# Optimization experiments

Measured on AMD Instinct MI355X. Metric: run time of the kernel, lower is better.

The kernel has to match this reference:

```python
import jax, jax.numpy as jnp
import numpy as np

N_NODES = 50000
N_RAND_EDGES = 800000
IN_FEATS = 128
NUM_HEADS = 4
OUT_FEATS = 32
NEG_SLOPE = 0.2


def setup_inputs() -> dict:
    key = jax.random.key(0)
    k_feat, k_src, k_dst, k_w, k_al, k_ar, k_b = jax.random.split(key, 7)
    feat = jax.random.normal(k_feat, (N_NODES, IN_FEATS), dtype=jnp.float32)
    # random edges + self-loops so every node has in-degree >= 1 (DGL requirement)
    src_r = jax.random.randint(k_src, (N_RAND_EDGES,), 0, N_NODES)
    dst_r = jax.random.randint(k_dst, (N_RAND_EDGES,), 0, N_NODES)
    loops = jnp.arange(N_NODES, dtype=src_r.dtype)
    src = jnp.concatenate([src_r, loops]).astype(jnp.int64)
    dst = jnp.concatenate([dst_r, loops]).astype(jnp.int64)
    W = jax.random.normal(k_w, (NUM_HEADS * OUT_FEATS, IN_FEATS), dtype=jnp.float32) * 0.05
    attn_l = jax.random.normal(k_al, (1, NUM_HEADS, OUT_FEATS), dtype=jnp.float32) * 0.1
    attn_r = jax.random.normal(k_ar, (1, NUM_HEADS, OUT_FEATS), dtype=jnp.float32) * 0.1
    bias = jnp.zeros((NUM_HEADS * OUT_FEATS,), dtype=jnp.float32)
    return {"feat": feat, "src": src, "dst": dst, "W": W,
            "attn_l": attn_l, "attn_r": attn_r, "bias": bias}


def _gat_forward(feat, src, dst, W, attn_l, attn_r, bias):
    n = feat.shape[0]
    # shared projection: in homogeneous path feat_src2 = feat_dst2 = fc(h)
    ft = (feat @ W.T).reshape(n, NUM_HEADS, OUT_FEATS)       # [N,H,D]
    el = jnp.sum(ft * attn_l, axis=-1)                        # [N,H]
    er = jnp.sum(ft * attn_r, axis=-1)                        # [N,H]
    e = el[src] + er[dst]                                     # [E,H]
    e = jnp.where(e > 0, e, NEG_SLOPE * e)                    # leaky_relu
    # edge softmax per destination node (numerically stable)
    m = jax.ops.segment_max(e, dst, num_segments=n)           # [N,H]
    ex = jnp.exp(e - m[dst])
    s = jax.ops.segment_sum(ex, dst, num_segments=n)          # [N,H]
    a = ex / s[dst]                                           # [E,H]
    # u_mul_e -> sum : attention-weighted aggregation
    msg1 = ft[src] * a[:, :, None]                            # [E,H,D]
    initial_ft = jax.ops.segment_sum(msg1, dst, num_segments=n)
    # u_mul_v -> sum : elementwise src*dst product aggregation
    msg2 = ft[src] * ft[dst]                                  # [E,H,D]
    add_ft = jax.ops.segment_sum(msg2, dst, num_segments=n)
    rst = initial_ft + add_ft + bias.reshape(1, NUM_HEADS, OUT_FEATS)
    return rst


def reference(feat, src, dst, W, attn_l, attn_r, bias):
    return _gat_forward(feat, src, dst, W, attn_l, attn_r, bias)
```

## Files before the change

### kernel.cpp

```cpp
#include <hip/hip_runtime.h>
#include <hip/hip_bf16.h>

#define IN_FEATS 128
#define HD 128
#define NEG_SLOPE 0.2f
#define LDR 128
#define CAP 64
#define BINW 256
#define CAPB 5120
#define NBLK 256
#define GPB 8
#define NPG 32
#define GM 64
#define LDA 136

typedef short s8v __attribute__((ext_vector_type(8)));
typedef float f4v __attribute__((ext_vector_type(4)));
typedef float f2v __attribute__((ext_vector_type(2)));

static __device__ __forceinline__ unsigned short f2bf(float f) {
    unsigned int u = __float_as_uint(f);
    unsigned int r = (u + 0x7FFFu + ((u >> 16) & 1u)) >> 16;
    return (unsigned short)r;
}
static __device__ __forceinline__ float bf2f(unsigned short h) {
    return __uint_as_float(((unsigned int)h) << 16);
}

static __device__ __forceinline__ void stage_W(unsigned short (*Wb)[LDA],
                                               const float* __restrict__ W) {
    const float4* W4 = (const float4*)W;
    for (int i = threadIdx.x; i < 4096; i += 256) {
        int r = i >> 5, q = i & 31;
        float4 w = W4[i];
        ushort4 o;
        o.x = f2bf(w.x); o.y = f2bf(w.y); o.z = f2bf(w.z); o.w = f2bf(w.w);
        *(ushort4*)&Wb[r][q * 4] = o;
    }
}

static __device__ __forceinline__ void gemm_tile(
        unsigned short (*Wb)[LDA], unsigned short (*Ab)[LDA],
        const float* __restrict__ feat, const float* __restrict__ attn_l,
        const float* __restrict__ attn_r, unsigned short* __restrict__ ftb,
        float* __restrict__ el, float* __restrict__ er, int N, int rbase) {
    const int tid  = threadIdx.x;
    const int wave = tid >> 6;
    const int lane = tid & 63;
    const int m    = lane & 15;
    const int quad = lane >> 4;

    const float4* F4 = (const float4*)feat;
    for (int i = tid; i < 2048; i += 256) {
        int r = i >> 5, q = i & 31;
        int gr = rbase + r;
        float4 v = (gr < N) ? F4[(size_t)gr * 32 + q]
                            : make_float4(0.f, 0.f, 0.f, 0.f);
        ushort4 o;
        o.x = f2bf(v.x); o.y = f2bf(v.y); o.z = f2bf(v.z); o.w = f2bf(v.w);
        *(ushort4*)&Ab[r][q * 4] = o;
    }
    __syncthreads();

    f4v acc[8];
#pragma unroll
    for (int t = 0; t < 8; ++t) acc[t] = (f4v){0.f, 0.f, 0.f, 0.f};

    const int arow = wave * 16 + m;
#pragma unroll
    for (int k0 = 0; k0 < 4; ++k0) {
        s8v a = *(const s8v*)&Ab[arow][k0 * 32 + quad * 8];
#pragma unroll
        for (int t = 0; t < 8; ++t) {
            s8v b = *(const s8v*)&Wb[t * 16 + m][k0 * 32 + quad * 8];
            acc[t] = __builtin_amdgcn_mfma_f32_16x16x32_bf16(a, b, acc[t], 0, 0, 0);
        }
    }

#pragma unroll
    for (int reg = 0; reg < 4; ++reg) {
        int gr = rbase + wave * 16 + quad * 4 + reg;
        if (gr < N) {
            unsigned short* dstrow = &ftb[(size_t)gr * LDR];
#pragma unroll
            for (int t = 0; t < 8; ++t)
                dstrow[t * 16 + m] = f2bf(acc[t][reg]);
        }
    }

    float al[8], ar[8];
#pragma unroll
    for (int t = 0; t < 8; ++t) {
        al[t] = attn_l[t * 16 + m];
        ar[t] = attn_r[t * 16 + m];
    }
#pragma unroll
    for (int h = 0; h < 4; ++h) {
#pragma unroll
        for (int reg = 0; reg < 4; ++reg) {
            float pl = acc[2 * h][reg] * al[2 * h] + acc[2 * h + 1][reg] * al[2 * h + 1];
            float pr = acc[2 * h][reg] * ar[2 * h] + acc[2 * h + 1][reg] * ar[2 * h + 1];
            pl += __shfl_xor(pl, 1); pr += __shfl_xor(pr, 1);
            pl += __shfl_xor(pl, 2); pr += __shfl_xor(pr, 2);
            pl += __shfl_xor(pl, 4); pr += __shfl_xor(pr, 4);
            pl += __shfl_xor(pl, 8); pr += __shfl_xor(pr, 8);
            if (m == 0) {
                int gr = rbase + wave * 16 + quad * 4 + reg;
                if (gr < N) {
                    el[gr * 4 + h] = pl;
                    er[gr * 4 + h] = pr;
                }
            }
        }
    }
}

__global__ __launch_bounds__(256) void count_gemm(
        const float* __restrict__ feat, const float* __restrict__ W,
        const float* __restrict__ attn_l, const float* __restrict__ attn_r,
        const int* __restrict__ dst, int E, int* __restrict__ cntBB,
        unsigned short* __restrict__ ftb, float* __restrict__ el,
        float* __restrict__ er, int N, int nbins) {
    __shared__ __align__(16) char smem[52224];
    const int tid = threadIdx.x;
    if (blockIdx.x < NBLK) {
        int* hist = (int*)smem;
        hist[tid] = 0;
        __syncthreads();
        const int chunk = (E + NBLK - 1) / NBLK;
        const int base = blockIdx.x * chunk;
        const int end = min(base + chunk, E);
        for (int i = base + tid; i < end; i += 256)
            atomicAdd(&hist[dst[i] >> 8], 1);
        __syncthreads();
        cntBB[blockIdx.x * 256 + tid] = hist[tid];
        return;
    }
    unsigned short (*Wb)[LDA] = (unsigned short (*)[LDA])smem;
    unsigned short (*Ab)[LDA] = (unsigned short (*)[LDA])(smem + 128 * LDA * 2);
    stage_W(Wb, W);
    gemm_tile(Wb, Ab, feat, attn_l, attn_r, ftb, el, er, N,
              (blockIdx.x - NBLK) * GM);
}

__global__ __launch_bounds__(256) void scan_scatter(
        const int* __restrict__ src, const int* __restrict__ dst, int E,
        const int* __restrict__ cntBB, unsigned int* __restrict__ binbuf,
        int nbins) {
    __shared__ int obase[256];
    __shared__ int lcnt[256];
    const int tid = threadIdx.x;
    const int bid = blockIdx.x;
    {
        int acc0 = 0, acc1 = 0, acc2 = 0, acc3 = 0;
        int acc4 = 0, acc5 = 0, acc6 = 0, acc7 = 0;
        int b = 0;
        for (; b + 8 <= bid; b += 8) {
            acc0 += cntBB[(b + 0) * 256 + tid];
            acc1 += cntBB[(b + 1) * 256 + tid];
            acc2 += cntBB[(b + 2) * 256 + tid];
            acc3 += cntBB[(b + 3) * 256 + tid];
            acc4 += cntBB[(b + 4) * 256 + tid];
            acc5 += cntBB[(b + 5) * 256 + tid];
            acc6 += cntBB[(b + 6) * 256 + tid];
            acc7 += cntBB[(b + 7) * 256 + tid];
        }
        for (; b < bid; ++b) acc0 += cntBB[b * 256 + tid];
        obase[tid] = ((acc0 + acc1) + (acc2 + acc3)) + ((acc4 + acc5) + (acc6 + acc7));
    }
    lcnt[tid] = 0;
    __syncthreads();
    const int chunk = (E + NBLK - 1) / NBLK;
    const int base = bid * chunk;
    const int end = min(base + chunk, E);
    for (int i = base + tid; i < end; i += 256) {
        int d = dst[i];
        int s = src[i];
        int bin = d >> 8;
        int r = atomicAdd(&lcnt[bin], 1);
        int idx = obase[bin] + r;
        if (idx < CAPB)
            binbuf[(size_t)bin * CAPB + idx] =
                ((unsigned int)(d & 255) << 16) | (unsigned int)s;
    }
}

__global__ __launch_bounds__(256) void bucket_agg(
        const unsigned int* __restrict__ binbuf, const int* __restrict__ cntBB,
        const unsigned short* __restrict__ ftb, const float* __restrict__ el,
        const float* __restrict__ er, const float* __restrict__ bias,
        float* __restrict__ out, int N, int nbins) {
    const int bin = blockIdx.x >> 3;
    const int g   = blockIdx.x & (GPB - 1);
    const int tid = threadIdx.x;

    __shared__ unsigned short lb[NPG * CAP];
    __shared__ int lcnt[NPG];
    __shared__ int red[256];

    if (tid < NPG) lcnt[tid] = 0;
    red[tid] = cntBB[tid * 256 + bin];
    __syncthreads();
    for (int s = 128; s > 0; s >>= 1) {
        if (tid < s) red[tid] += red[tid + s];
        __syncthreads();
    }
    const int total = min(red[0], CAPB);

    const unsigned int* bb = binbuf + (size_t)bin * CAPB;
    for (int i = tid; i < total; i += 256) {
        unsigned int v = bb[i];
        int dl = (int)(v >> 16);
        if ((dl >> 5) == g) {
            int ln = dl & (NPG - 1);
            int pos = atomicAdd(&lcnt[ln], 1);
            if (pos < CAP) lb[(ln << 6) + pos] = (unsigned short)(v & 0xFFFFu);
        }
    }
    __syncthreads();

    const int wave = tid >> 6;
    const int lane = tid & 63;
    const int h  = lane >> 4;
    const int c0 = lane * 2;

    for (int ln = wave; ln < NPG; ln += 4) {
        const int n = (bin << 8) + (g << 5) + ln;
        if (n >= N) break;

        const float ern = er[(n << 2) + h];
        unsigned int tn = *(const unsigned int*)(ftb + ((size_t)n << 7) + c0);
        f2v ftn; ftn.x = __uint_as_float(tn << 16);
        ftn.y = __uint_as_float(tn & 0xFFFF0000u);

        const int deg = min(lcnt[ln], CAP);
        const unsigned short* eb = &lb[ln << 6];

        f2v accA = (f2v){0.f, 0.f};
        f2v accB = (f2v){0.f, 0.f};
        float sum = 0.f;

        int i = 0;
        for (; i + 4 <= deg; i += 4) {
            ushort4 s4 = *(const ushort4*)&eb[i];
            int sA = s4.x, sB = s4.y, sC = s4.z, sD = s4.w;
            float eA = el[(sA << 2) + h];
            float eB = el[(sB << 2) + h];
            float eC = el[(sC << 2) + h];
            float eD = el[(sD << 2) + h];
            unsigned int fA = *(const unsigned int*)(ftb + ((size_t)sA << 7) + c0);
            unsigned int fB = *(const unsigned int*)(ftb + ((size_t)sB << 7) + c0);
            unsigned int fC = *(const unsigned int*)(ftb + ((size_t)sC << 7) + c0);
            unsigned int fD = *(const unsigned int*)(ftb + ((size_t)sD << 7) + c0);
            eA += ern; eB += ern; eC += ern; eD += ern;
            eA = fmaxf(eA, NEG_SLOPE * eA);
            eB = fmaxf(eB, NEG_SLOPE * eB);
            eC = fmaxf(eC, NEG_SLOPE * eC);
            eD = fmaxf(eD, NEG_SLOPE * eD);
            float xA = __expf(eA), xB = __expf(eB);
            float xC = __expf(eC), xD = __expf(eD);
            f2v ffA; ffA.x = __uint_as_float(fA << 16); ffA.y = __uint_as_float(fA & 0xFFFF0000u);
            f2v ffB; ffB.x = __uint_as_float(fB << 16); ffB.y = __uint_as_float(fB & 0xFFFF0000u);
            f2v ffC; ffC.x = __uint_as_float(fC << 16); ffC.y = __uint_as_float(fC & 0xFFFF0000u);
            f2v ffD; ffD.x = __uint_as_float(fD << 16); ffD.y = __uint_as_float(fD & 0xFFFF0000u);
            sum += (xA + xB) + (xC + xD);
            accA += xA * ffA;
            accA += xB * ffB;
            accA += xC * ffC;
            accA += xD * ffD;
            accB += ffA + ffB;
            accB += ffC + ffD;
        }
        for (; i < deg; ++i) {
            int s = eb[i];
            float e = el[(s << 2) + h] + ern;
            e = fmaxf(e, NEG_SLOPE * e);
            float x = __expf(e);
            unsigned int f = *(const unsigned int*)(ftb + ((size_t)s << 7) + c0);
            f2v ff; ff.x = __uint_as_float(f << 16); ff.y = __uint_as_float(f & 0xFFFF0000u);
            sum += x;
            accA += x * ff;
            accB += ff;
        }

        float inv = 1.f / sum;
        f2v o = accA * inv + ftn * accB;
        float2 ov;
        ov.x = o.x + bias[c0];
        ov.y = o.y + bias[c0 + 1];
        *(float2*)(out + (size_t)n * HD + c0) = ov;
    }
}

extern "C" void kernel_launch(void* const* d_in, const int* in_sizes, int n_in,
                              void* d_out, int out_size, void* d_ws, size_t ws_size,
                              hipStream_t stream) {
    const float* feat   = (const float*)d_in[0];
    const int*   src    = (const int*)d_in[1];
    const int*   dst    = (const int*)d_in[2];
    const float* W      = (const float*)d_in[3];
    const float* attn_l = (const float*)d_in[4];
    const float* attn_r = (const float*)d_in[5];
    const float* bias   = (const float*)d_in[6];

    const int N = in_sizes[0] / IN_FEATS;
    const int E = in_sizes[1];
    const int nbins = (N + BINW - 1) / BINW;

    char* p = (char*)d_ws;
    auto alloc = [&](size_t bytes) {
        char* q = p;
        p += (bytes + 255) & ~(size_t)255;
        return q;
    };
    unsigned short* ftb  = (unsigned short*)alloc((size_t)N * LDR * 2);
    float* el      = (float*)alloc((size_t)N * 4 * 4);
    float* er      = (float*)alloc((size_t)N * 4 * 4);
    unsigned int* binbuf = (unsigned int*)alloc((size_t)nbins * CAPB * 4);
    int*   cntBB   = (int*)alloc((size_t)NBLK * 256 * 4);

    const int gemm_blocks = (N + GM - 1) / GM;
    count_gemm<<<NBLK + gemm_blocks, 256, 0, stream>>>(
        feat, W, attn_l, attn_r, dst, E, cntBB, ftb, el, er, N, nbins);

    scan_scatter<<<NBLK, 256, 0, stream>>>(src, dst, E, cntBB, binbuf, nbins);

    bucket_agg<<<nbins * GPB, 256, 0, stream>>>(binbuf, cntBB, ftb, el, er,
                                                bias, (float*)d_out, N, nbins);
}
```

Before: 168.5 us.

## Software-pipeline edge gathers in batches of 8 with padded dummy node

Pads each destination's neighbor list to a multiple of 8 using a dummy node whose features are zero and whose logit is very negative. The aggregation loop then prefetches the next 8 edges while processing the current 8. Per-bin totals are computed once in the scatter kernel instead of reduced in every aggregation block, and the per-block histogram is stored as 16-bit. The aim is more memory-level parallelism on the random gathers, at the cost of extra register pressure and some wasted padded work.

```diff
diff --git a/kernel.cpp b/kernel.cpp
--- a/kernel.cpp
+++ b/kernel.cpp
@@ -22,9 +22,6 @@
     unsigned int u = __float_as_uint(f);
     unsigned int r = (u + 0x7FFFu + ((u >> 16) & 1u)) >> 16;
     return (unsigned short)r;
-}
-static __device__ __forceinline__ float bf2f(unsigned short h) {
-    return __uint_as_float(((unsigned int)h) << 16);
 }
 
 static __device__ __forceinline__ void stage_W(unsigned short (*Wb)[LDA],
@@ -118,7 +115,7 @@
 __global__ __launch_bounds__(256) void count_gemm(
         const float* __restrict__ feat, const float* __restrict__ W,
         const float* __restrict__ attn_l, const float* __restrict__ attn_r,
-        const int* __restrict__ dst, int E, int* __restrict__ cntBB,
+        const int* __restrict__ dst, int E, unsigned short* __restrict__ cntBB,
         unsigned short* __restrict__ ftb, float* __restrict__ el,
         float* __restrict__ er, int N, int nbins) {
     __shared__ __align__(16) char smem[52224];
@@ -133,8 +130,12 @@
         for (int i = base + tid; i < end; i += 256)
             atomicAdd(&hist[dst[i] >> 8], 1);
         __syncthreads();
-        cntBB[blockIdx.x * 256 + tid] = hist[tid];
+        cntBB[blockIdx.x * 256 + tid] = (unsigned short)hist[tid];
         return;
+    }
+    if (blockIdx.x == NBLK) {
+        if (tid < 64) ((unsigned int*)(ftb + (size_t)N * LDR))[tid] = 0u;
+        if (tid < 4)  el[N * 4 + tid] = -1e30f;
     }
     unsigned short (*Wb)[LDA] = (unsigned short (*)[LDA])smem;
     unsigned short (*Ab)[LDA] = (unsigned short (*)[LDA])(smem + 128 * LDA * 2);
@@ -145,8 +146,8 @@
 
 __global__ __launch_bounds__(256) void scan_scatter(
         const int* __restrict__ src, const int* __restrict__ dst, int E,
-        const int* __restrict__ cntBB, unsigned int* __restrict__ binbuf,
-        int nbins) {
+        const unsigned short* __restrict__ cntBB, unsigned int* __restrict__ binbuf,
+        int* __restrict__ binTotal, int nbins) {
     __shared__ int obase[256];
     __shared__ int lcnt[256];
     const int tid = threadIdx.x;
@@ -183,10 +184,50 @@
             binbuf[(size_t)bin * CAPB + idx] =
                 ((unsigned int)(d & 255) << 16) | (unsigned int)s;
     }
-}
-
-__global__ __launch_bounds__(256) void bucket_agg(
-        const unsigned int* __restrict__ binbuf, const int* __restrict__ cntBB,
+    __syncthreads();
+    if (bid == NBLK - 1)
+        binTotal[tid] = obase[tid] + lcnt[tid];
+}
+
+struct B8 {
+    float e[8];
+    unsigned int f[8];
+};
+
+static __device__ __forceinline__ B8 loadb(const unsigned short* eb, int base,
+                                           const float* __restrict__ el,
+                                           const unsigned int* __restrict__ ftbu,
+                                           int h, int lane) {
+    B8 r;
+    ushort4 q0 = *(const ushort4*)&eb[base];
+    ushort4 q1 = *(const ushort4*)&eb[base + 4];
+    unsigned int id[8] = {q0.x, q0.y, q0.z, q0.w, q1.x, q1.y, q1.z, q1.w};
+#pragma unroll
+    for (int j = 0; j < 8; ++j) {
+        r.e[j] = el[(id[j] << 2) + h];
+        r.f[j] = ftbu[(id[j] << 6) + lane];
+    }
+    return r;
+}
+
+static __device__ __forceinline__ void procb(const B8& v, float ern, float& sum,
+                                             f2v& accA, f2v& accB) {
+#pragma unroll
+    for (int j = 0; j < 8; ++j) {
+        float e = v.e[j] + ern;
+        e = fmaxf(e, NEG_SLOPE * e);
+        float x = __expf(e);
+        f2v ff;
+        ff.x = __uint_as_float(v.f[j] << 16);
+        ff.y = __uint_as_float(v.f[j] & 0xFFFF0000u);
+        sum += x;
+        accA += x * ff;
+        accB += ff;
+    }
+}
+
+__global__ __launch_bounds__(256, 8) void bucket_agg(
+        const unsigned int* __restrict__ binbuf, const int* __restrict__ binTotal,
         const unsigned short* __restrict__ ftb, const float* __restrict__ el,
         const float* __restrict__ er, const float* __restrict__ bias,
         float* __restrict__ out, int N, int nbins) {
@@ -196,16 +237,11 @@
 
     __shared__ unsigned short lb[NPG * CAP];
     __shared__ int lcnt[NPG];
-    __shared__ int red[256];
 
     if (tid < NPG) lcnt[tid] = 0;
-    red[tid] = cntBB[tid * 256 + bin];
-    __syncthreads();
-    for (int s = 128; s > 0; s >>= 1) {
-        if (tid < s) red[tid] += red[tid + s];
-        __syncthreads();
-    }
-    const int total = min(red[0], CAPB);
+    __syncthreads();
+
+    const int total = min(binTotal[bin], CAPB);
 
     const unsigned int* bb = binbuf + (size_t)bin * CAPB;
     for (int i = tid; i < total; i += 256) {
@@ -218,69 +254,50 @@
         }
     }
     __syncthreads();
+    if (tid < NPG) {
+        int c = min(lcnt[tid], CAP);
+        int cp = (c + 7) & ~7;
+        for (int k = c; k < cp; ++k) lb[(tid << 6) + k] = (unsigned short)N;
+        lcnt[tid] = cp;
+    }
+    __syncthreads();
 
     const int wave = tid >> 6;
     const int lane = tid & 63;
     const int h  = lane >> 4;
     const int c0 = lane * 2;
+    const unsigned int* ftbu = (const unsigned int*)ftb;
 
     for (int ln = wave; ln < NPG; ln += 4) {
         const int n = (bin << 8) + (g << 5) + ln;
         if (n >= N) break;
 
         const float ern = er[(n << 2) + h];
-        unsigned int tn = *(const unsigned int*)(ftb + ((size_t)n << 7) + c0);
+        unsigned int tn = ftbu[((unsigned int)n << 6) + lane];
         f2v ftn; ftn.x = __uint_as_float(tn << 16);
         ftn.y = __uint_as_float(tn & 0xFFFF0000u);
 
-        const int deg = min(lcnt[ln], CAP);
+        const int nb = lcnt[ln] >> 3;
         const unsigned short* eb = &lb[ln << 6];
 
         f2v accA = (f2v){0.f, 0.f};
         f2v accB = (f2v){0.f, 0.f};
         float sum = 0.f;
 
-        int i = 0;
-        for (; i + 4 <= deg; i += 4) {
-            ushort4 s4 = *(const ushort4*)&eb[i];
-            int sA = s4.x, sB = s4.y, sC = s4.z, sD = s4.w;
-            float eA = el[(sA << 2) + h];
-            float eB = el[(sB << 2) + h];
-            float eC = el[(sC << 2) + h];
-            float eD = el[(sD << 2) + h];
-            unsigned int fA = *(const unsigned int*)(ftb + ((size_t)sA << 7) + c0);
-            unsigned int fB = *(const unsigned int*)(ftb + ((size_t)sB << 7) + c0);
-            unsigned int fC = *(const unsigned int*)(ftb + ((size_t)sC << 7) + c0);
-            unsigned int fD = *(const unsigned int*)(ftb + ((size_t)sD << 7) + c0);
-            eA += ern; eB += ern; eC += ern; eD += ern;
-            eA = fmaxf(eA, NEG_SLOPE * eA);
-            eB = fmaxf(eB, NEG_SLOPE * eB);
-            eC = fmaxf(eC, NEG_SLOPE * eC);
-            eD = fmaxf(eD, NEG_SLOPE * eD);
-            float xA = __expf(eA), xB = __expf(eB);
-            float xC = __expf(eC), xD = __expf(eD);
-            f2v ffA; ffA.x = __uint_as_float(fA << 16); ffA.y = __uint_as_float(fA & 0xFFFF0000u);
-            f2v ffB; ffB.x = __uint_as_float(fB << 16); ffB.y = __uint_as_float(fB & 0xFFFF0000u);
-            f2v ffC; ffC.x = __uint_as_float(fC << 16); ffC.y = __uint_as_float(fC & 0xFFFF0000u);
-            f2v ffD; ffD.x = __uint_as_float(fD << 16); ffD.y = __uint_as_float(fD & 0xFFFF0000u);
-            sum += (xA + xB) + (xC + xD);
-            accA += xA * ffA;
-            accA += xB * ffB;
-            accA += xC * ffC;
-            accA += xD * ffD;
-            accB += ffA + ffB;
-            accB += ffC + ffD;
-        }
-        for (; i < deg; ++i) {
-            int s = eb[i];
-            float e = el[(s << 2) + h] + ern;
-            e = fmaxf(e, NEG_SLOPE * e);
-            float x = __expf(e);
-            unsigned int f = *(const unsigned int*)(ftb + ((size_t)s << 7) + c0);
-            f2v ff; ff.x = __uint_as_float(f << 16); ff.y = __uint_as_float(f & 0xFFFF0000u);
-            sum += x;
-            accA += x * ff;
-            accB += ff;
+        if (nb > 0) {
+            B8 A = loadb(eb, 0, el, ftbu, h, lane);
+            int b = 0;
+            while (true) {
+                if (b + 1 < nb) {
+                    B8 Bn = loadb(eb, (b + 1) << 3, el, ftbu, h, lane);
+                    procb(A, ern, sum, accA, accB);
+                    A = Bn;
+                    ++b;
+                } else {
+                    procb(A, ern, sum, accA, accB);
+                    break;
+                }
+            }
         }
 
         float inv = 1.f / sum;
@@ -313,18 +330,20 @@
         p += (bytes + 255) & ~(size_t)255;
         return q;
     };
-    unsigned short* ftb  = (unsigned short*)alloc((size_t)N * LDR * 2);
-    float* el      = (float*)alloc((size_t)N * 4 * 4);
-    float* er      = (float*)alloc((size_t)N * 4 * 4);
+    unsigned short* ftb  = (unsigned short*)alloc((size_t)(N + 1) * LDR * 2);
+    float* el      = (float*)alloc((size_t)(N + 1) * 4 * 4);
+    float* er      = (float*)alloc((size_t)(N + 1) * 4 * 4);
     unsigned int* binbuf = (unsigned int*)alloc((size_t)nbins * CAPB * 4);
-    int*   cntBB   = (int*)alloc((size_t)NBLK * 256 * 4);
+    unsigned short* cntBB = (unsigned short*)alloc((size_t)NBLK * 256 * 2);
+    int* binTotal  = (int*)alloc((size_t)nbins * 4);
 
     const int gemm_blocks = (N + GM - 1) / GM;
     count_gemm<<<NBLK + gemm_blocks, 256, 0, stream>>>(
         feat, W, attn_l, attn_r, dst, E, cntBB, ftb, el, er, N, nbins);
 
-    scan_scatter<<<NBLK, 256, 0, stream>>>(src, dst, E, cntBB, binbuf, nbins);
-
-    bucket_agg<<<nbins * GPB, 256, 0, stream>>>(binbuf, cntBB, ftb, el, er,
+    scan_scatter<<<NBLK, 256, 0, stream>>>(src, dst, E, cntBB, binbuf,
+                                           binTotal, nbins);
+
+    bucket_agg<<<nbins * GPB, 256, 0, stream>>>(binbuf, binTotal, ftb, el, er,
                                                 bias, (float*)d_out, N, nbins);
 }
```

After: 169.7 us. Within noise of the previous version (+0.7%).

## Precompute bin totals in scatter, halve nodes per aggregation block, shrink counts

Applied to the files above, without the earlier changes.

The last scatter block now writes per-bin totals, so each aggregation block reads one value instead of reducing 256 counts from cntBB. Per-block histogram counts are stored as 16-bit values to cut traffic in the scan. The aggregation grid doubles to 16 groups per bin with 16 nodes each, which raises parallelism but means every bin's edge list is scanned twice as many times. Gather indexing switches to 32-bit unsigned word offsets to simplify address arithmetic.

```diff
diff --git a/kernel.cpp b/kernel.cpp
--- a/kernel.cpp
+++ b/kernel.cpp
@@ -9,8 +9,8 @@
 #define BINW 256
 #define CAPB 5120
 #define NBLK 256
-#define GPB 8
-#define NPG 32
+#define GPB 16
+#define NPG 16
 #define GM 64
 #define LDA 136
 
@@ -22,9 +22,6 @@
     unsigned int u = __float_as_uint(f);
     unsigned int r = (u + 0x7FFFu + ((u >> 16) & 1u)) >> 16;
     return (unsigned short)r;
-}
-static __device__ __forceinline__ float bf2f(unsigned short h) {
-    return __uint_as_float(((unsigned int)h) << 16);
 }
 
 static __device__ __forceinline__ void stage_W(unsigned short (*Wb)[LDA],
@@ -118,7 +115,7 @@
 __global__ __launch_bounds__(256) void count_gemm(
         const float* __restrict__ feat, const float* __restrict__ W,
         const float* __restrict__ attn_l, const float* __restrict__ attn_r,
-        const int* __restrict__ dst, int E, int* __restrict__ cntBB,
+        const int* __restrict__ dst, int E, unsigned short* __restrict__ cntBB,
         unsigned short* __restrict__ ftb, float* __restrict__ el,
         float* __restrict__ er, int N, int nbins) {
     __shared__ __align__(16) char smem[52224];
@@ -133,7 +130,7 @@
         for (int i = base + tid; i < end; i += 256)
             atomicAdd(&hist[dst[i] >> 8], 1);
         __syncthreads();
-        cntBB[blockIdx.x * 256 + tid] = hist[tid];
+        cntBB[blockIdx.x * 256 + tid] = (unsigned short)hist[tid];
         return;
     }
     unsigned short (*Wb)[LDA] = (unsigned short (*)[LDA])smem;
@@ -145,8 +142,8 @@
 
 __global__ __launch_bounds__(256) void scan_scatter(
         const int* __restrict__ src, const int* __restrict__ dst, int E,
-        const int* __restrict__ cntBB, unsigned int* __restrict__ binbuf,
-        int nbins) {
+        const unsigned short* __restrict__ cntBB, unsigned int* __restrict__ binbuf,
+        int* __restrict__ binTotal, int nbins) {
     __shared__ int obase[256];
     __shared__ int lcnt[256];
     const int tid = threadIdx.x;
@@ -183,35 +180,33 @@
             binbuf[(size_t)bin * CAPB + idx] =
                 ((unsigned int)(d & 255) << 16) | (unsigned int)s;
     }
+    __syncthreads();
+    if (bid == NBLK - 1)
+        binTotal[tid] = obase[tid] + lcnt[tid];
 }
 
 __global__ __launch_bounds__(256) void bucket_agg(
-        const unsigned int* __restrict__ binbuf, const int* __restrict__ cntBB,
+        const unsigned int* __restrict__ binbuf, const int* __restrict__ binTotal,
         const unsigned short* __restrict__ ftb, const float* __restrict__ el,
         const float* __restrict__ er, const float* __restrict__ bias,
         float* __restrict__ out, int N, int nbins) {
-    const int bin = blockIdx.x >> 3;
+    const int bin = blockIdx.x >> 4;
     const int g   = blockIdx.x & (GPB - 1);
     const int tid = threadIdx.x;
 
     __shared__ unsigned short lb[NPG * CAP];
     __shared__ int lcnt[NPG];
-    __shared__ int red[256];
 
     if (tid < NPG) lcnt[tid] = 0;
-    red[tid] = cntBB[tid * 256 + bin];
-    __syncthreads();
-    for (int s = 128; s > 0; s >>= 1) {
-        if (tid < s) red[tid] += red[tid + s];
-        __syncthreads();
-    }
-    const int total = min(red[0], CAPB);
+    __syncthreads();
+
+    const int total = min(binTotal[bin], CAPB);
 
     const unsigned int* bb = binbuf + (size_t)bin * CAPB;
     for (int i = tid; i < total; i += 256) {
         unsigned int v = bb[i];
         int dl = (int)(v >> 16);
-        if ((dl >> 5) == g) {
+        if ((dl >> 4) == g) {
             int ln = dl & (NPG - 1);
             int pos = atomicAdd(&lcnt[ln], 1);
             if (pos < CAP) lb[(ln << 6) + pos] = (unsigned short)(v & 0xFFFFu);
@@ -223,13 +218,14 @@
     const int lane = tid & 63;
     const int h  = lane >> 4;
     const int c0 = lane * 2;
+    const unsigned int* ftbu = (const unsigned int*)ftb;
 
     for (int ln = wave; ln < NPG; ln += 4) {
-        const int n = (bin << 8) + (g << 5) + ln;
+        const int n = (bin << 8) + (g << 4) + ln;
         if (n >= N) break;
 
         const float ern = er[(n << 2) + h];
-        unsigned int tn = *(const unsigned int*)(ftb + ((size_t)n << 7) + c0);
+        unsigned int tn = ftbu[((unsigned int)n << 6) + lane];
         f2v ftn; ftn.x = __uint_as_float(tn << 16);
         ftn.y = __uint_as_float(tn & 0xFFFF0000u);
 
@@ -243,15 +239,15 @@
         int i = 0;
         for (; i + 4 <= deg; i += 4) {
             ushort4 s4 = *(const ushort4*)&eb[i];
-            int sA = s4.x, sB = s4.y, sC = s4.z, sD = s4.w;
+            unsigned int sA = s4.x, sB = s4.y, sC = s4.z, sD = s4.w;
             float eA = el[(sA << 2) + h];
             float eB = el[(sB << 2) + h];
             float eC = el[(sC << 2) + h];
             float eD = el[(sD << 2) + h];
-            unsigned int fA = *(const unsigned int*)(ftb + ((size_t)sA << 7) + c0);
-            unsigned int fB = *(const unsigned int*)(ftb + ((size_t)sB << 7) + c0);
-            unsigned int fC = *(const unsigned int*)(ftb + ((size_t)sC << 7) + c0);
-            unsigned int fD = *(const unsigned int*)(ftb + ((size_t)sD << 7) + c0);
+            unsigned int fA = ftbu[(sA << 6) + lane];
+            unsigned int fB = ftbu[(sB << 6) + lane];
+            unsigned int fC = ftbu[(sC << 6) + lane];
+            unsigned int fD = ftbu[(sD << 6) + lane];
             eA += ern; eB += ern; eC += ern; eD += ern;
             eA = fmaxf(eA, NEG_SLOPE * eA);
             eB = fmaxf(eB, NEG_SLOPE * eB);
@@ -272,11 +268,11 @@
             accB += ffC + ffD;
         }
         for (; i < deg; ++i) {
-            int s = eb[i];
+            unsigned int s = eb[i];
             float e = el[(s << 2) + h] + ern;
             e = fmaxf(e, NEG_SLOPE * e);
             float x = __expf(e);
-            unsigned int f = *(const unsigned int*)(ftb + ((size_t)s << 7) + c0);
+            unsigned int f = ftbu[(s << 6) + lane];
             f2v ff; ff.x = __uint_as_float(f << 16); ff.y = __uint_as_float(f & 0xFFFF0000u);
             sum += x;
             accA += x * ff;
@@ -317,14 +313,16 @@
     float* el      = (float*)alloc((size_t)N * 4 * 4);
     float* er      = (float*)alloc((size_t)N * 4 * 4);
     unsigned int* binbuf = (unsigned int*)alloc((size_t)nbins * CAPB * 4);
-    int*   cntBB   = (int*)alloc((size_t)NBLK * 256 * 4);
+    unsigned short* cntBB = (unsigned short*)alloc((size_t)NBLK * 256 * 2);
+    int* binTotal  = (int*)alloc(256 * 4);
 
     const int gemm_blocks = (N + GM - 1) / GM;
     count_gemm<<<NBLK + gemm_blocks, 256, 0, stream>>>(
         feat, W, attn_l, attn_r, dst, E, cntBB, ftb, el, er, N, nbins);
 
-    scan_scatter<<<NBLK, 256, 0, stream>>>(src, dst, E, cntBB, binbuf, nbins);
-
-    bucket_agg<<<nbins * GPB, 256, 0, stream>>>(binbuf, cntBB, ftb, el, er,
+    scan_scatter<<<NBLK, 256, 0, stream>>>(src, dst, E, cntBB, binbuf,
+                                           binTotal, nbins);
+
+    bucket_agg<<<nbins * GPB, 256, 0, stream>>>(binbuf, binTotal, ftb, el, er,
                                                 bias, (float*)d_out, N, nbins);
 }
```

After: 170.2 us. About the same (+1.0%).
